# Kernel tuning notes

Hardware: AMD Instinct MI355X
Metric: run time of the kernel (lower is better)

Reference implementation:

```python
import jax, jax.numpy as jnp
import numpy as np

L, B, D_MODEL, N_STATE = 512, 32, 256, 16
DT_RANK = 16          # ceil(d_model / 16)
D_INNER = D_MODEL     # EXPAND = 1 (required for code self-consistency)


def setup_inputs() -> dict:
    key = jax.random.key(0)
    ks = jax.random.split(key, 6)
    return {
        "position_features": jax.random.normal(ks[0], (L, B, D_MODEL), jnp.float32),
        "flow_features": jax.random.normal(ks[1], (L, B, D_MODEL), jnp.float32),
        "h_state": jnp.zeros((B, D_INNER, N_STATE), jnp.float32),
        "x_proj_w": jax.random.normal(ks[2], (DT_RANK + 2 * N_STATE, D_INNER), jnp.float32) / np.sqrt(D_INNER).astype(np.float32),
        "dt_proj_w": jax.random.normal(ks[3], (D_INNER, DT_RANK), jnp.float32) / np.sqrt(DT_RANK).astype(np.float32),
        "dt_proj_b": jax.random.normal(ks[4], (D_INNER,), jnp.float32) * 0.01,
        "A_log": jnp.log(jnp.broadcast_to(jnp.arange(1, N_STATE + 1, dtype=jnp.float32), (D_INNER, N_STATE))),
        "D_param": jnp.ones((D_INNER,), jnp.float32),
        "out_proj_w": jax.random.normal(ks[5], (D_MODEL, D_INNER), jnp.float32) / np.sqrt(D_INNER).astype(np.float32),
    }


def _forward(position_features, flow_features, h_state,
             x_proj_w, dt_proj_w, dt_proj_b, A_log, D_param, out_proj_w):
    # permute (L, B, d) -> (B, L, d), matching forward()'s permute(1,0,2)
    u = jnp.transpose(position_features, (1, 0, 2))      # (b, l, d_in)
    flow = jnp.transpose(flow_features, (1, 0, 2))       # (b, l, d_in)

    # input-dependent delta, B, C from flow features
    x_dbl = flow @ x_proj_w.T                            # (b, l, dt_rank + 2n)
    delta, Bm, Cm = jnp.split(x_dbl, [DT_RANK, DT_RANK + N_STATE], axis=-1)
    delta = jax.nn.softplus(delta @ dt_proj_w.T + dt_proj_b)   # (b, l, d_in)

    A = -jnp.exp(A_log)                                  # (d_in, n)
    deltaA = jnp.exp(jnp.einsum('bld,dn->bldn', delta, A))         # (b,l,d,n)
    deltaB_u = jnp.einsum('bld,bln,bld->bldn', delta, Bm, u)       # (b,l,d,n)

    # sequential selective scan over l via lax.scan
    dA_t = jnp.swapaxes(deltaA, 0, 1)                    # (l, b, d, n)
    dBu_t = jnp.swapaxes(deltaB_u, 0, 1)                 # (l, b, d, n)
    C_t = jnp.swapaxes(Cm, 0, 1)                         # (l, b, n)

    def step(h, xs):
        dA, dBu, c = xs
        h = dA * h + dBu                                 # (b, d, n)
        y = jnp.einsum('bdn,bn->bd', h, c)               # (b, d)
        return h, y

    h_final, ys = jax.lax.scan(step, h_state, (dA_t, dBu_t, C_t))
    y = jnp.swapaxes(ys, 0, 1)                           # (b, l, d_in)
    y = y + u * D_param                                  # skip connection

    out = y @ out_proj_w.T                               # (b, l, d_model)
    return out.reshape(out.shape[0], -1), h_final        # flatten(1)


def reference(position_features, flow_features, h_state,
              x_proj_w, dt_proj_w, dt_proj_b, A_log, D_param, out_proj_w):
    return _forward(position_features, flow_features, h_state,
                    x_proj_w, dt_proj_w, dt_proj_b, A_log, D_param, out_proj_w)
```

## Files before the change

kernel.cpp:

```cpp
#include <hip/hip_runtime.h>
#include <hip/hip_bf16.h>

#define LL 512
#define BB 32
#define DD 256
#define NS 16
#define RK 16
#define CH 32
#define LC 16

typedef __attribute__((ext_vector_type(8))) short bf16x8;
typedef __attribute__((ext_vector_type(8))) _Float16 f16x8;
typedef __attribute__((ext_vector_type(4))) float f32x4;

#define LD16(dst, src, off) { \
  float4 _v0 = *reinterpret_cast<const float4*>(&(src)[(off)]); \
  float4 _v1 = *reinterpret_cast<const float4*>(&(src)[(off)+4]); \
  float4 _v2 = *reinterpret_cast<const float4*>(&(src)[(off)+8]); \
  float4 _v3 = *reinterpret_cast<const float4*>(&(src)[(off)+12]); \
  dst[0]=_v0.x; dst[1]=_v0.y; dst[2]=_v0.z; dst[3]=_v0.w; \
  dst[4]=_v1.x; dst[5]=_v1.y; dst[6]=_v1.z; dst[7]=_v1.w; \
  dst[8]=_v2.x; dst[9]=_v2.y; dst[10]=_v2.z; dst[11]=_v2.w; \
  dst[12]=_v3.x; dst[13]=_v3.y; dst[14]=_v3.z; dst[15]=_v3.w; }

static __device__ __forceinline__ unsigned short f2bf(float x) {
    __hip_bfloat16 h = __float2bfloat16(x);
    return *reinterpret_cast<unsigned short*>(&h);
}

static __device__ __forceinline__ f16x8 ld_cvt_f16(const float* p) {
    float4 lo = *reinterpret_cast<const float4*>(p);
    float4 hi = *reinterpret_cast<const float4*>(p + 4);
    f16x8 r;
    r[0] = (_Float16)lo.x; r[1] = (_Float16)lo.y; r[2] = (_Float16)lo.z; r[3] = (_Float16)lo.w;
    r[4] = (_Float16)hi.x; r[5] = (_Float16)hi.y; r[6] = (_Float16)hi.z; r[7] = (_Float16)hi.w;
    return r;
}

__global__ __launch_bounds__(256) void k0_wbf(
    const float* __restrict__ W, unsigned short* __restrict__ Wbf)
{
    int i = (blockIdx.x * 256 + threadIdx.x) * 4;
    float4 v = *reinterpret_cast<const float4*>(&W[i]);
    ushort4 o;
    o.x = f2bf(v.x); o.y = f2bf(v.y); o.z = f2bf(v.z); o.w = f2bf(v.w);
    *reinterpret_cast<ushort4*>(&Wbf[i]) = o;
}

__global__ __launch_bounds__(256) void k0_atab(
    const float* __restrict__ A_log, float* __restrict__ atab)
{
    int i = blockIdx.x * 256 + threadIdx.x;
    atab[i] = -__expf(A_log[i]) * 1.44269504f;
}

__global__ __launch_bounds__(256) void k1_fused(
    const float* __restrict__ flow,
    const float* __restrict__ xw,
    const float* __restrict__ dtw,
    const float* __restrict__ dtb,
    float* __restrict__ delta,
    float* __restrict__ Bm,
    float* __restrict__ Cm)
{
    __shared__ float sx16[4][16][17];
    int wave = threadIdx.x >> 6;
    int lane = threadIdx.x & 63;
    int rl = lane & 15, kb = lane >> 4;
    int rowbase = blockIdx.x * 64 + wave * 16;
    int arow = rowbase + rl;
    int b = arow >> 9, l = arow & 511;
    const float* abase = &flow[(l * BB + b) * DD];

    f32x4 acc[3] = {};
    #pragma unroll
    for (int ks = 0; ks < 8; ++ks) {
        int k0 = ks * 32 + kb * 8;
        f16x8 af = ld_cvt_f16(abase + k0);
        #pragma unroll
        for (int j = 0; j < 3; ++j) {
            f16x8 bfr = ld_cvt_f16(&xw[(j * 16 + rl) * DD + k0]);
            acc[j] = __builtin_amdgcn_mfma_f32_16x16x32_f16(af, bfr, acc[j], 0, 0, 0);
        }
    }
    #pragma unroll
    for (int reg = 0; reg < 4; ++reg) {
        int row = rowbase + kb * 4 + reg;
        Bm[(size_t)row * NS + rl] = acc[1][reg];
        Cm[(size_t)row * NS + rl] = acc[2][reg];
        sx16[wave][kb * 4 + reg][rl] = acc[0][reg];
    }
    __syncthreads();

    f16x8 a2;
    if (kb < 2) {
        #pragma unroll
        for (int j = 0; j < 8; ++j)
            a2[j] = (_Float16)sx16[wave][rl][kb * 8 + j];
    } else {
        #pragma unroll
        for (int j = 0; j < 8; ++j) a2[j] = (_Float16)0.f;
    }

    #pragma unroll 4
    for (int m = 0; m < 16; ++m) {
        f16x8 b2;
        if (kb < 2) {
            float4 lo = *reinterpret_cast<const float4*>(&dtw[(m * 16 + rl) * RK + kb * 8]);
            float4 hi = *reinterpret_cast<const float4*>(&dtw[(m * 16 + rl) * RK + kb * 8 + 4]);
            b2[0] = (_Float16)lo.x; b2[1] = (_Float16)lo.y; b2[2] = (_Float16)lo.z; b2[3] = (_Float16)lo.w;
            b2[4] = (_Float16)hi.x; b2[5] = (_Float16)hi.y; b2[6] = (_Float16)hi.z; b2[7] = (_Float16)hi.w;
        } else {
            #pragma unroll
            for (int j = 0; j < 8; ++j) b2[j] = (_Float16)0.f;
        }
        f32x4 acc2 = {};
        acc2 = __builtin_amdgcn_mfma_f32_16x16x32_f16(a2, b2, acc2, 0, 0, 0);
        int d = m * 16 + rl;
        float bias = dtb[d];
        #pragma unroll
        for (int reg = 0; reg < 4; ++reg) {
            float s = acc2[reg] + bias;
            float sp = fmaxf(s, 0.f) + log1pf(__expf(-fabsf(s)));
            delta[(size_t)(rowbase + kb * 4 + reg) * DD + d] = sp;
        }
    }
}

__global__ __launch_bounds__(512) void k2A(
    const float* __restrict__ u_pos,
    const float* __restrict__ atab,
    const float* __restrict__ Dp,
    float* __restrict__ delta,
    const float* __restrict__ Bm,
    const float* __restrict__ Cm,
    float* __restrict__ ypart,
    float* __restrict__ hfin,
    float* __restrict__ sfin)
{
    int tid = threadIdx.x;
    int b  = blockIdx.x >> 4;
    int dt = blockIdx.x & 15;
    int dl = tid & 15, c = tid >> 4;
    int d  = dt * 16 + dl;
    int l0 = c * LC;

    float a[NS];
    LD16(a, atab, d * NS);
    float Dd = Dp[d];

    float* dp = delta + ((size_t)b * LL + l0) * DD + d;
    const float* up = u_pos + ((size_t)l0 * BB + b) * DD + d;
    const float* Bp = Bm + ((size_t)b * LL + l0) * NS;
    const float* Cp = Cm + ((size_t)b * LL + l0) * NS;
    float* yp = ypart + ((size_t)b * LL + l0) * DD + d;

    float h[NS];
    #pragma unroll
    for (int n = 0; n < NS; ++n) h[n] = 0.f;
    float s = 0.f;

    for (int l = 0; l < LC; ++l) {
        float dlt = dp[l * DD];
        float uv  = up[l * BB * DD];
        float Bv[NS], Cv[NS];
        LD16(Bv, Bp, l * NS);
        LD16(Cv, Cp, l * NS);
        s += dlt;
        float du = dlt * uv;
        float acc = uv * Dd;
        #pragma unroll
        for (int n = 0; n < NS; ++n) {
            float dA = exp2f(dlt * a[n]);
            h[n] = fmaf(dA, h[n], du * Bv[n]);
            acc = fmaf(h[n], Cv[n], acc);
        }
        yp[l * DD] = acc;
        dp[l * DD] = s;
    }

    size_t o = (((size_t)b * CH + c) * DD + d);
    sfin[o] = s;
    #pragma unroll
    for (int n = 0; n < NS; n += 4)
        *reinterpret_cast<float4*>(&hfin[o * NS + n]) =
            make_float4(h[n], h[n+1], h[n+2], h[n+3]);
}

__global__ __launch_bounds__(256) void k2B(
    const float* __restrict__ h0,
    const float* __restrict__ atab,
    const float* __restrict__ sfin,
    float* __restrict__ hfin,
    float* __restrict__ h_out)
{
    int t = blockIdx.x * 256 + threadIdx.x;
    int n = t & 15, d = (t >> 4) & 255, b = t >> 12;
    float an = atab[d * NS + n];
    float s = h0[t];
    for (int c = 0; c < CH; ++c) {
        size_t o = ((size_t)b * CH + c) * DD + d;
        float sf = sfin[o];
        size_t oh = o * NS + n;
        float hp = hfin[oh];
        hfin[oh] = s;
        s = fmaf(exp2f(an * sf), s, hp);
    }
    h_out[t] = s;
}

__global__ __launch_bounds__(256) void k2C(
    const float* __restrict__ atab,
    const float* __restrict__ Slocal,
    const float* __restrict__ Cm,
    const float* __restrict__ hfin,
    const float* __restrict__ ypart,
    unsigned short* __restrict__ ybf)
{
    int d = threadIdx.x;
    int b = blockIdx.x >> 9;
    int l = blockIdx.x & 511;
    int c = l >> 4;

    float a[NS], hin[NS], Cv[NS];
    LD16(a, atab, d * NS);
    LD16(hin, hfin, (((size_t)b * CH + c) * DD + d) * NS);
    LD16(Cv, Cm, ((size_t)b * LL + l) * NS);

    size_t idx = ((size_t)b * LL + l) * DD + d;
    float sS = Slocal[idx];
    float acc = ypart[idx];
    #pragma unroll
    for (int n = 0; n < NS; ++n)
        acc = fmaf(exp2f(a[n] * sS), Cv[n] * hin[n], acc);
    ybf[idx] = f2bf(acc);
}

__global__ __launch_bounds__(256) void k3_mfma(
    const unsigned short* __restrict__ Ybf,
    const unsigned short* __restrict__ Wbf,
    float* __restrict__ Out)
{
    int wave = threadIdx.x >> 6;
    int lane = threadIdx.x & 63;
    int row0 = (blockIdx.x >> 1) * 32 + (wave >> 1) * 16;
    int col0 = (blockIdx.x & 1) * 128 + (wave & 1) * 64;
    int rl = lane & 15, kb = lane >> 4;

    f32x4 acc[4] = {};
    bf16x8 af, bf[4], afn, bfn[4];

    af = *reinterpret_cast<const bf16x8*>(&Ybf[(size_t)(row0 + rl) * DD + kb * 8]);
    #pragma unroll
    for (int j = 0; j < 4; ++j)
        bf[j] = *reinterpret_cast<const bf16x8*>(&Wbf[(size_t)(col0 + j * 16 + rl) * DD + kb * 8]);

    #pragma unroll
    for (int ks = 0; ks < 8; ++ks) {
        int kn = (ks + 1) * 32 + kb * 8;
        if (ks < 7) {
            afn = *reinterpret_cast<const bf16x8*>(&Ybf[(size_t)(row0 + rl) * DD + kn]);
            #pragma unroll
            for (int j = 0; j < 4; ++j)
                bfn[j] = *reinterpret_cast<const bf16x8*>(&Wbf[(size_t)(col0 + j * 16 + rl) * DD + kn]);
        }
        #pragma unroll
        for (int j = 0; j < 4; ++j)
            acc[j] = __builtin_amdgcn_mfma_f32_16x16x32_bf16(af, bf[j], acc[j], 0, 0, 0);
        af = afn;
        #pragma unroll
        for (int j = 0; j < 4; ++j) bf[j] = bfn[j];
    }

    #pragma unroll
    for (int j = 0; j < 4; ++j)
        #pragma unroll
        for (int reg = 0; reg < 4; ++reg)
            Out[(size_t)(row0 + kb * 4 + reg) * DD + col0 + j * 16 + rl] = acc[j][reg];
}

extern "C" void kernel_launch(void* const* d_in, const int* in_sizes, int n_in,
                              void* d_out, int out_size, void* d_ws, size_t ws_size,
                              hipStream_t stream) {
    const float* pos  = (const float*)d_in[0];
    const float* flow = (const float*)d_in[1];
    const float* h0   = (const float*)d_in[2];
    const float* xw   = (const float*)d_in[3];
    const float* dtw  = (const float*)d_in[4];
    const float* dtb  = (const float*)d_in[5];
    const float* alog = (const float*)d_in[6];
    const float* dpar = (const float*)d_in[7];
    const float* ow   = (const float*)d_in[8];

    float* out = (float*)d_out;

    float* ws    = (float*)d_ws;
    float* delta = ws;
    float* Bmw   = ws + 4194304;
    float* Cmw   = ws + 4456448;
    float* ypart = ws + 4718592;
    float* hfin  = ws + 8912896;
    float* sfin  = ws + 13107200;
    float* atab  = ws + 13369344;
    unsigned short* ybf = (unsigned short*)(ws + 13373440);
    unsigned short* wbf = (unsigned short*)(ws + 15470592);

    float* h_out = out + 32 * 512 * 256;

    k0_wbf  <<<64,    256, 0, stream>>>(ow, wbf);
    k0_atab <<<16,    256, 0, stream>>>(alog, atab);
    k1_fused<<<256,   256, 0, stream>>>(flow, xw, dtw, dtb, delta, Bmw, Cmw);
    k2A     <<<512,   512, 0, stream>>>(pos, atab, dpar, delta, Bmw, Cmw, ypart, hfin, sfin);
    k2B     <<<512,   256, 0, stream>>>(h0, atab, sfin, hfin, h_out);
    k2C     <<<16384, 256, 0, stream>>>(atab, delta, Cmw, hfin, ypart, ybf);
    k3_mfma <<<1024,  256, 0, stream>>>(ybf, wbf, out);
}
```

Baseline: 226.5 us.

## Transpose chunk-state layout to d-contiguous and restructure scan fix-up kernels

Stores the per-chunk scan states as [b][c][n][d] and adds a transposed A table, so stores in the chunked scan and loads in the carry-propagation and correction kernels are coalesced across d. The correction kernel now handles one whole chunk per block and loops over its 16 timesteps, loading A and the carried-in state once instead of once per timestep, with 1024 blocks instead of 16384. The chunked scan also prefetches the next timestep's delta, u, B and C, and gets an occupancy hint in its launch bounds. The cost is higher register pressure in the scan kernel and fewer, longer-running blocks in the correction kernel.

```diff
diff --git a/kernel.cpp b/kernel.cpp
--- a/kernel.cpp
+++ b/kernel.cpp
@@ -23,6 +23,8 @@
   dst[8]=_v2.x; dst[9]=_v2.y; dst[10]=_v2.z; dst[11]=_v2.w; \
   dst[12]=_v3.x; dst[13]=_v3.y; dst[14]=_v3.z; dst[15]=_v3.w; }
 
+#define CP16(dst, src) { _Pragma("unroll") for (int _i = 0; _i < 16; ++_i) dst[_i] = src[_i]; }
+
 static __device__ __forceinline__ unsigned short f2bf(float x) {
     __hip_bfloat16 h = __float2bfloat16(x);
     return *reinterpret_cast<unsigned short*>(&h);
@@ -48,10 +50,13 @@
 }
 
 __global__ __launch_bounds__(256) void k0_atab(
-    const float* __restrict__ A_log, float* __restrict__ atab)
+    const float* __restrict__ A_log, float* __restrict__ atab, float* __restrict__ atabT)
 {
     int i = blockIdx.x * 256 + threadIdx.x;
-    atab[i] = -__expf(A_log[i]) * 1.44269504f;
+    int d = i >> 4, n = i & 15;
+    float v = -__expf(A_log[i]) * 1.44269504f;
+    atab[i] = v;
+    atabT[n * DD + d] = v;
 }
 
 __global__ __launch_bounds__(256) void k1_fused(
@@ -127,7 +132,7 @@
     }
 }
 
-__global__ __launch_bounds__(512) void k2A(
+__global__ __launch_bounds__(512, 4) void k2A(
     const float* __restrict__ u_pos,
     const float* __restrict__ atab,
     const float* __restrict__ Dp,
@@ -160,12 +165,19 @@
     for (int n = 0; n < NS; ++n) h[n] = 0.f;
     float s = 0.f;
 
+    float dlt = dp[0], uv = up[0];
+    float Bv[NS], Cv[NS];
+    LD16(Bv, Bp, 0);
+    LD16(Cv, Cp, 0);
+
     for (int l = 0; l < LC; ++l) {
-        float dlt = dp[l * DD];
-        float uv  = up[l * BB * DD];
-        float Bv[NS], Cv[NS];
-        LD16(Bv, Bp, l * NS);
-        LD16(Cv, Cp, l * NS);
+        int lp = (l + 1 < LC) ? l + 1 : l;
+        float dlt_n = dp[lp * DD];
+        float uv_n  = up[lp * BB * DD];
+        float Bn[NS], Cn[NS];
+        LD16(Bn, Bp, lp * NS);
+        LD16(Cn, Cp, lp * NS);
+
         s += dlt;
         float du = dlt * uv;
         float acc = uv * Dd;
@@ -177,40 +189,42 @@
         }
         yp[l * DD] = acc;
         dp[l * DD] = s;
-    }
-
-    size_t o = (((size_t)b * CH + c) * DD + d);
-    sfin[o] = s;
-    #pragma unroll
-    for (int n = 0; n < NS; n += 4)
-        *reinterpret_cast<float4*>(&hfin[o * NS + n]) =
-            make_float4(h[n], h[n+1], h[n+2], h[n+3]);
+
+        dlt = dlt_n; uv = uv_n;
+        CP16(Bv, Bn); CP16(Cv, Cn);
+    }
+
+    sfin[((size_t)b * CH + c) * DD + d] = s;
+    #pragma unroll
+    for (int n = 0; n < NS; ++n)
+        hfin[(((size_t)b * CH + c) * NS + n) * DD + d] = h[n];
 }
 
 __global__ __launch_bounds__(256) void k2B(
     const float* __restrict__ h0,
-    const float* __restrict__ atab,
+    const float* __restrict__ atabT,
     const float* __restrict__ sfin,
     float* __restrict__ hfin,
     float* __restrict__ h_out)
 {
-    int t = blockIdx.x * 256 + threadIdx.x;
-    int n = t & 15, d = (t >> 4) & 255, b = t >> 12;
-    float an = atab[d * NS + n];
-    float s = h0[t];
+    int d = threadIdx.x;
+    int b = blockIdx.x >> 4;
+    int n = blockIdx.x & 15;
+    float an = atabT[n * DD + d];
+    float s = h0[((size_t)b * DD + d) * NS + n];
+    #pragma unroll 4
     for (int c = 0; c < CH; ++c) {
-        size_t o = ((size_t)b * CH + c) * DD + d;
-        float sf = sfin[o];
-        size_t oh = o * NS + n;
+        float sf = sfin[((size_t)b * CH + c) * DD + d];
+        size_t oh = (((size_t)b * CH + c) * NS + n) * DD + d;
         float hp = hfin[oh];
         hfin[oh] = s;
         s = fmaf(exp2f(an * sf), s, hp);
     }
-    h_out[t] = s;
+    h_out[((size_t)b * DD + d) * NS + n] = s;
 }
 
 __global__ __launch_bounds__(256) void k2C(
-    const float* __restrict__ atab,
+    const float* __restrict__ atabT,
     const float* __restrict__ Slocal,
     const float* __restrict__ Cm,
     const float* __restrict__ hfin,
@@ -218,22 +232,32 @@
     unsigned short* __restrict__ ybf)
 {
     int d = threadIdx.x;
-    int b = blockIdx.x >> 9;
-    int l = blockIdx.x & 511;
-    int c = l >> 4;
-
-    float a[NS], hin[NS], Cv[NS];
-    LD16(a, atab, d * NS);
-    LD16(hin, hfin, (((size_t)b * CH + c) * DD + d) * NS);
-    LD16(Cv, Cm, ((size_t)b * LL + l) * NS);
-
-    size_t idx = ((size_t)b * LL + l) * DD + d;
-    float sS = Slocal[idx];
-    float acc = ypart[idx];
-    #pragma unroll
-    for (int n = 0; n < NS; ++n)
-        acc = fmaf(exp2f(a[n] * sS), Cv[n] * hin[n], acc);
-    ybf[idx] = f2bf(acc);
+    int b = blockIdx.x >> 5;
+    int c = blockIdx.x & 31;
+    int l0 = c * LC;
+
+    float a[NS], hin[NS];
+    #pragma unroll
+    for (int n = 0; n < NS; ++n) {
+        a[n]   = atabT[n * DD + d];
+        hin[n] = hfin[(((size_t)b * CH + c) * NS + n) * DD + d];
+    }
+
+    size_t base = ((size_t)b * LL + l0) * DD + d;
+    const float* CpB = Cm + ((size_t)b * LL + l0) * NS;
+
+    #pragma unroll 2
+    for (int l = 0; l < LC; ++l) {
+        float Cv[NS];
+        LD16(Cv, CpB, l * NS);
+        size_t idx = base + (size_t)l * DD;
+        float sS = Slocal[idx];
+        float acc = ypart[idx];
+        #pragma unroll
+        for (int n = 0; n < NS; ++n)
+            acc = fmaf(exp2f(a[n] * sS), Cv[n] * hin[n], acc);
+        ybf[idx] = f2bf(acc);
+    }
 }
 
 __global__ __launch_bounds__(256) void k3_mfma(
@@ -302,16 +326,17 @@
     float* hfin  = ws + 8912896;
     float* sfin  = ws + 13107200;
     float* atab  = ws + 13369344;
-    unsigned short* ybf = (unsigned short*)(ws + 13373440);
-    unsigned short* wbf = (unsigned short*)(ws + 15470592);
+    float* atabT = ws + 13373440;
+    unsigned short* ybf = (unsigned short*)(ws + 13377536);
+    unsigned short* wbf = (unsigned short*)(ws + 15474688);
 
     float* h_out = out + 32 * 512 * 256;
 
-    k0_wbf  <<<64,    256, 0, stream>>>(ow, wbf);
-    k0_atab <<<16,    256, 0, stream>>>(alog, atab);
-    k1_fused<<<256,   256, 0, stream>>>(flow, xw, dtw, dtb, delta, Bmw, Cmw);
-    k2A     <<<512,   512, 0, stream>>>(pos, atab, dpar, delta, Bmw, Cmw, ypart, hfin, sfin);
-    k2B     <<<512,   256, 0, stream>>>(h0, atab, sfin, hfin, h_out);
-    k2C     <<<16384, 256, 0, stream>>>(atab, delta, Cmw, hfin, ypart, ybf);
-    k3_mfma <<<1024,  256, 0, stream>>>(ybf, wbf, out);
-}
+    k0_wbf  <<<64,   256, 0, stream>>>(ow, wbf);
+    k0_atab <<<16,   256, 0, stream>>>(alog, atab, atabT);
+    k1_fused<<<256,  256, 0, stream>>>(flow, xw, dtw, dtb, delta, Bmw, Cmw);
+    k2A     <<<512,  512, 0, stream>>>(pos, atab, dpar, delta, Bmw, Cmw, ypart, hfin, sfin);
+    k2B     <<<512,  256, 0, stream>>>(h0, atabT, sfin, hfin, h_out);
+    k2C     <<<1024, 256, 0, stream>>>(atabT, delta, Cmw, hfin, ypart, ybf);
+    k3_mfma <<<1024, 256, 0, stream>>>(ybf, wbf, out);
+}
```

After: 214.9 us. 1.05x faster.
